# Optimization experiments

Measured on AMD Instinct MI355X. Metric: run time of the kernel, lower is better.

## Reference

```python
import jax, jax.numpy as jnp
import numpy as np

B, N, F_IN, F_OUT = 4, 4096, 64, 64
ALPHA = 0.2  # LeakyReLU negative slope
NEG_INF = -9e15


def setup_inputs() -> dict:
    key = jax.random.key(0)
    k1, k2, k3, k4 = jax.random.split(key, 4)
    h = jax.random.normal(k1, (B, N, F_IN), dtype=jnp.float32)
    adj = jax.random.randint(k2, (B, N, N), 0, 2, dtype=jnp.int32)
    # xavier_uniform-like init (gain 1.414)
    lim_w = 1.414 * np.sqrt(6.0 / (F_IN + F_OUT))
    W = jax.random.uniform(k3, (F_IN, F_OUT), dtype=jnp.float32, minval=-lim_w, maxval=lim_w)
    lim_a = 1.414 * np.sqrt(6.0 / (2 * F_OUT + 1))
    a = jax.random.uniform(k4, (2 * F_OUT, 1), dtype=jnp.float32, minval=-lim_a, maxval=lim_a)
    return {"h": h, "adj": adj, "W": W, "a": a}


def reference(h, adj, W, a):
    # Wh: [B, N, F_out]
    Wh = jnp.matmul(h, W)
    a1 = a[:F_OUT, 0]   # [F_out]
    a2 = a[F_OUT:, 0]   # [F_out]
    # e[b,i,j] = LeakyReLU(Wh[b,i].a1 + Wh[b,j].a2)  (decomposed, avoids O(N^2*2F) concat)
    ei = jnp.einsum('bnf,f->bn', Wh, a1)  # source term
    ej = jnp.einsum('bnf,f->bn', Wh, a2)  # target term
    e = ei[:, :, None] + ej[:, None, :]   # [B, N, N]
    e = jnp.where(e > 0, e, ALPHA * e)    # LeakyReLU
    att = jnp.where(adj > 0, e, NEG_INF)
    att = jax.nn.softmax(att, axis=-1)
    h_prime = jnp.matmul(att, Wh)         # [B, N, F_out]
    return jax.nn.elu(h_prime)
```

## Files before the change

### kernel.cpp

```cpp
#include <hip/hip_runtime.h>
#include <stdint.h>

#define N_NODES 4096
#define F_DIM   64
#define LRELU_ALPHA 0.2f

typedef _Float16 f16;
typedef __attribute__((ext_vector_type(8))) _Float16 half8;
typedef __attribute__((ext_vector_type(4))) float f32x4;

__global__ __launch_bounds__(256) void gat_pp(
    const float* __restrict__ h, const float* __restrict__ W,
    const float* __restrict__ a, const int* __restrict__ adj,
    float* __restrict__ ei, float* __restrict__ ej,
    f16* __restrict__ whB, float* __restrict__ blockmax,
    uint32_t* __restrict__ bits)
{
  __shared__ float sh_h[4][F_DIM];
  __shared__ f16 tile[F_DIM][16];
  __shared__ float wmax[4];
  const int t = threadIdx.x, w = t >> 6, lane = t & 63;

  if (blockIdx.x >= 1024) {
    const int r = blockIdx.x - 1024;
    const int* row = adj + (size_t)r * N_NODES;
    const int jw0 = w * 1024;

    int v[16];
#pragma unroll
    for (int p = 0; p < 16; ++p)
      v[p] = row[jw0 + p * 64 + lane];

#pragma unroll
    for (int p = 0; p < 16; ++p) {
      const unsigned long long m = __ballot(v[p] > 0);
      if (lane == 0)
        *(uint64_t*)(bits + (size_t)r * 128 + ((jw0 + p * 64) >> 5)) = m;
    }
    return;
  }

  const int n0 = blockIdx.x * 16;
  const int b  = n0 >> 12;
  const int nl0 = n0 & (N_NODES - 1);

  float wcol[F_DIM];
#pragma unroll
  for (int k = 0; k < F_DIM; ++k) wcol[k] = W[k * F_DIM + lane];
  const float a1 = a[lane], a2 = a[F_DIM + lane];

  float runmax = -3e38f;
  for (int r = 0; r < 4; ++r) {
    const int loc = w * 4 + r;
    const int n = n0 + loc;
    const float hv = h[(size_t)n * F_DIM + lane];
    sh_h[w][lane] = hv;
    float wh = 0.f;
#pragma unroll
    for (int k = 0; k < F_DIM; k += 4) {
      const float4 hb = *(const float4*)(&sh_h[w][k]);
      wh = fmaf(hb.x, wcol[k + 0], wh);
      wh = fmaf(hb.y, wcol[k + 1], wh);
      wh = fmaf(hb.z, wcol[k + 2], wh);
      wh = fmaf(hb.w, wcol[k + 3], wh);
    }
    float s1 = wh * a1, s2 = wh * a2;
#pragma unroll
    for (int off = 32; off; off >>= 1) {
      s1 += __shfl_xor(s1, off);
      s2 += __shfl_xor(s2, off);
    }
    if (lane == 0) { ei[n] = s1; ej[n] = s2; }
    runmax = fmaxf(runmax, s2);
    tile[lane][loc] = (f16)wh;
  }
  if (lane == 0) wmax[w] = runmax;
  __syncthreads();

  {
    const int jc = nl0 >> 5;
    const int q0 = (nl0 >> 3) & 3;
    const int fc = t >> 6;
    const int r6 = t & 63;
    const int qp = r6 >> 5;
    const int m  = (r6 >> 1) & 15;
    const int xh = (t & 1) * 4;
    const int loc = qp * 8 + xh;
    f16* dst = whB + (((size_t)(b * 128 + jc)) * 4 + fc) * 512
                   + ((q0 + qp) * 16 + m) * 8 + xh;
    *(uint2*)dst = *(const uint2*)(&tile[fc * 16 + m][loc]);
  }
  if (t == 0)
    blockmax[blockIdx.x] =
        fmaxf(fmaxf(wmax[0], wmax[1]), fmaxf(wmax[2], wmax[3]));
}

__global__ __launch_bounds__(512, 6) void gat_attn(
    const uint32_t* __restrict__ bits, const float* __restrict__ ei,
    const float* __restrict__ ej, const f16* __restrict__ whB,
    const float* __restrict__ blockmax, float* __restrict__ out)
{
  __shared__ float num_lds[8][16][F_DIM];
  __shared__ float den_lds[8][16];

  const int t = threadIdx.x, w = t >> 6, lane = t & 63;
  const int quad = lane >> 4, m = lane & 15;
  const int b  = blockIdx.x >> 8;
  const int i0 = (blockIdx.x & 255) * 16;
  const int i  = i0 + m;
  const int rowg = b * N_NODES + i;

  float maxej;
  {
    const float4 v = *(const float4*)(blockmax + b * 256 + lane * 4);
    maxej = fmaxf(fmaxf(v.x, v.y), fmaxf(v.z, v.w));
#pragma unroll
    for (int off = 32; off; off >>= 1)
      maxej = fmaxf(maxej, __shfl_xor(maxej, off));
  }

  const float ei_s = ei[rowg];
  float bnd = ei_s + maxej;
  bnd = fmaxf(bnd, LRELU_ALPHA * bnd);
  const float c1 = ei_s - bnd;
  const float c2 = LRELU_ALPHA * ei_s - bnd;

  const float* ejb     = ej + b * N_NODES;
  const uint32_t* bitrow = bits + (size_t)rowg * 128 + w * 16;
  const f16* whw = whB + ((size_t)(b * 128 + w * 16)) * 2048 + lane * 8;

  f32x4 acc[4] = {{0.f,0.f,0.f,0.f},{0.f,0.f,0.f,0.f},
                  {0.f,0.f,0.f,0.f},{0.f,0.f,0.f,0.f}};
  float den = 0.f;
  const int jbase = w * (N_NODES / 8);

  for (int jo = 0; jo < 4; ++jo) {
    const uint4 dq = *(const uint4*)(bitrow + jo * 4);
    const uint32_t dws[4] = {dq.x, dq.y, dq.z, dq.w};

#pragma unroll
    for (int ji = 0; ji < 4; ++ji) {
      const int jc = jo * 4 + ji;
      const int jk = jbase + jc * 32 + quad * 8;
      const uint32_t dw = dws[ji];

      float ejA[8];
      *(float4*)(&ejA[0]) = *(const float4*)(ejb + jk);
      *(float4*)(&ejA[4]) = *(const float4*)(ejb + jk + 4);

      const f16* wjc = whw + (size_t)jc * 2048;
      half8 bf[4];
#pragma unroll
      for (int fc = 0; fc < 4; ++fc)
        bf[fc] = *(const half8*)(wjc + fc * 512);

      half8 pa;
#pragma unroll
      for (int x = 0; x < 8; ++x) {
        const float arg = fmaxf(ejA[x] + c1, fmaf(LRELU_ALPHA, ejA[x], c2));
        const float p =
            ((dw >> (quad * 8 + x)) & 1u) ? __expf(arg) : 0.f;
        pa[x] = (f16)p;
        den += (float)pa[x];
      }

#pragma unroll
      for (int fc = 0; fc < 4; ++fc)
        acc[fc] = __builtin_amdgcn_mfma_f32_16x16x32_f16(pa, bf[fc], acc[fc], 0, 0, 0);
    }
  }

  den += __shfl_xor(den, 16);
  den += __shfl_xor(den, 32);
  if (lane < 16) den_lds[w][lane] = den;

#pragma unroll
  for (int fc = 0; fc < 4; ++fc)
#pragma unroll
    for (int rg = 0; rg < 4; ++rg)
      num_lds[w][quad * 4 + rg][fc * 16 + m] = acc[fc][rg];
  __syncthreads();

#pragma unroll
  for (int k = 0; k < 2; ++k) {
    const int idx = k * 512 + t;
    const int il = idx >> 6, f = idx & 63;
    float num = 0.f, d = 0.f;
#pragma unroll
    for (int ww = 0; ww < 8; ++ww) {
      num += num_lds[ww][il][f];
      d   += den_lds[ww][il];
    }
    float v = (d > 0.f) ? (num / d) : 0.f;
    v = (v > 0.f) ? v : expm1f(v);
    out[((size_t)(b * N_NODES + i0 + il)) * F_DIM + f] = v;
  }
}

extern "C" void kernel_launch(void* const* d_in, const int* in_sizes, int n_in,
                              void* d_out, int out_size, void* d_ws, size_t ws_size,
                              hipStream_t stream) {
  const float* h   = (const float*)d_in[0];
  const int*   adj = (const int*)d_in[1];
  const float* W   = (const float*)d_in[2];
  const float* a   = (const float*)d_in[3];
  float* out = (float*)d_out;

  char* ws = (char*)d_ws;
  float*    ei       = (float*)ws;
  float*    ej       = (float*)(ws + 65536);
  float*    blockmax = (float*)(ws + 131072);
  f16*      whB      = (f16*)(ws + 135168);
  uint32_t* bits     = (uint32_t*)(ws + 2232320);

  hipLaunchKernelGGL(gat_pp, dim3(17408), dim3(256), 0, stream,
                     h, W, a, adj, ei, ej, whB, blockmax, bits);
  hipLaunchKernelGGL(gat_attn, dim3(1024), dim3(512), 0, stream,
                     bits, ei, ej, whB, blockmax, out);
}
```

Baseline: 400.2 us.

## Process 32 rows per attention block and interleave projection with adjacency packing

```diff
diff --git a/kernel.cpp b/kernel.cpp
--- a/kernel.cpp
+++ b/kernel.cpp
@@ -20,9 +20,11 @@
   __shared__ f16 tile[F_DIM][16];
   __shared__ float wmax[4];
   const int t = threadIdx.x, w = t >> 6, lane = t & 63;
-
-  if (blockIdx.x >= 1024) {
-    const int r = blockIdx.x - 1024;
+  const int bid = blockIdx.x;
+  const int pid = bid / 17;
+
+  if (bid % 17 != 0) {
+    const int r = bid - 1 - pid;
     const int* row = adj + (size_t)r * N_NODES;
     const int jw0 = w * 1024;
 
@@ -40,7 +42,7 @@
     return;
   }
 
-  const int n0 = blockIdx.x * 16;
+  const int n0 = pid * 16;
   const int b  = n0 >> 12;
   const int nl0 = n0 & (N_NODES - 1);
 
@@ -91,24 +93,24 @@
     *(uint2*)dst = *(const uint2*)(&tile[fc * 16 + m][loc]);
   }
   if (t == 0)
-    blockmax[blockIdx.x] =
+    blockmax[pid] =
         fmaxf(fmaxf(wmax[0], wmax[1]), fmaxf(wmax[2], wmax[3]));
 }
 
-__global__ __launch_bounds__(512, 6) void gat_attn(
+__global__ __launch_bounds__(512, 4) void gat_attn(
     const uint32_t* __restrict__ bits, const float* __restrict__ ei,
     const float* __restrict__ ej, const f16* __restrict__ whB,
     const float* __restrict__ blockmax, float* __restrict__ out)
 {
-  __shared__ float num_lds[8][16][F_DIM];
-  __shared__ float den_lds[8][16];
+  __shared__ float num_lds[8][32][F_DIM];
+  __shared__ float den_lds[8][32];
 
   const int t = threadIdx.x, w = t >> 6, lane = t & 63;
   const int quad = lane >> 4, m = lane & 15;
-  const int b  = blockIdx.x >> 8;
-  const int i0 = (blockIdx.x & 255) * 16;
-  const int i  = i0 + m;
-  const int rowg = b * N_NODES + i;
+  const int b  = blockIdx.x >> 7;
+  const int i0 = (blockIdx.x & 127) * 32;
+  const int rowg0 = b * N_NODES + i0 + m;
+  const int rowg1 = rowg0 + 16;
 
   float maxej;
   {
@@ -119,30 +121,37 @@
       maxej = fmaxf(maxej, __shfl_xor(maxej, off));
   }
 
-  const float ei_s = ei[rowg];
-  float bnd = ei_s + maxej;
-  bnd = fmaxf(bnd, LRELU_ALPHA * bnd);
-  const float c1 = ei_s - bnd;
-  const float c2 = LRELU_ALPHA * ei_s - bnd;
-
-  const float* ejb     = ej + b * N_NODES;
-  const uint32_t* bitrow = bits + (size_t)rowg * 128 + w * 16;
+  const float ei0 = ei[rowg0], ei1 = ei[rowg1];
+  float bnd0 = ei0 + maxej;
+  bnd0 = fmaxf(bnd0, LRELU_ALPHA * bnd0);
+  float bnd1 = ei1 + maxej;
+  bnd1 = fmaxf(bnd1, LRELU_ALPHA * bnd1);
+  const float c10 = ei0 - bnd0, c20 = LRELU_ALPHA * ei0 - bnd0;
+  const float c11 = ei1 - bnd1, c21 = LRELU_ALPHA * ei1 - bnd1;
+
+  const float* ejb = ej + b * N_NODES;
+  const uint32_t* bitrow0 = bits + (size_t)rowg0 * 128 + w * 16;
+  const uint32_t* bitrow1 = bits + (size_t)rowg1 * 128 + w * 16;
   const f16* whw = whB + ((size_t)(b * 128 + w * 16)) * 2048 + lane * 8;
 
-  f32x4 acc[4] = {{0.f,0.f,0.f,0.f},{0.f,0.f,0.f,0.f},
-                  {0.f,0.f,0.f,0.f},{0.f,0.f,0.f,0.f}};
-  float den = 0.f;
+  f32x4 acc0[4] = {{0.f,0.f,0.f,0.f},{0.f,0.f,0.f,0.f},
+                   {0.f,0.f,0.f,0.f},{0.f,0.f,0.f,0.f}};
+  f32x4 acc1[4] = {{0.f,0.f,0.f,0.f},{0.f,0.f,0.f,0.f},
+                   {0.f,0.f,0.f,0.f},{0.f,0.f,0.f,0.f}};
+  float den0 = 0.f, den1 = 0.f;
   const int jbase = w * (N_NODES / 8);
 
   for (int jo = 0; jo < 4; ++jo) {
-    const uint4 dq = *(const uint4*)(bitrow + jo * 4);
-    const uint32_t dws[4] = {dq.x, dq.y, dq.z, dq.w};
+    const uint4 dq0 = *(const uint4*)(bitrow0 + jo * 4);
+    const uint4 dq1 = *(const uint4*)(bitrow1 + jo * 4);
+    const uint32_t dws0[4] = {dq0.x, dq0.y, dq0.z, dq0.w};
+    const uint32_t dws1[4] = {dq1.x, dq1.y, dq1.z, dq1.w};
 
 #pragma unroll
     for (int ji = 0; ji < 4; ++ji) {
       const int jc = jo * 4 + ji;
       const int jk = jbase + jc * 32 + quad * 8;
-      const uint32_t dw = dws[ji];
+      const uint32_t dw0 = dws0[ji], dw1 = dws1[ji];
 
       float ejA[8];
       *(float4*)(&ejA[0]) = *(const float4*)(ejb + jk);
@@ -154,35 +163,48 @@
       for (int fc = 0; fc < 4; ++fc)
         bf[fc] = *(const half8*)(wjc + fc * 512);
 
-      half8 pa;
+      half8 pa0, pa1;
 #pragma unroll
       for (int x = 0; x < 8; ++x) {
-        const float arg = fmaxf(ejA[x] + c1, fmaf(LRELU_ALPHA, ejA[x], c2));
-        const float p =
-            ((dw >> (quad * 8 + x)) & 1u) ? __expf(arg) : 0.f;
-        pa[x] = (f16)p;
-        den += (float)pa[x];
+        const float e = ejA[x];
+        const float g0 = fmaxf(e + c10, fmaf(LRELU_ALPHA, e, c20));
+        const float g1 = fmaxf(e + c11, fmaf(LRELU_ALPHA, e, c21));
+        const float p0 = ((dw0 >> (quad * 8 + x)) & 1u) ? __expf(g0) : 0.f;
+        const float p1 = ((dw1 >> (quad * 8 + x)) & 1u) ? __expf(g1) : 0.f;
+        pa0[x] = (f16)p0;
+        pa1[x] = (f16)p1;
+        den0 += (float)pa0[x];
+        den1 += (float)pa1[x];
       }
 
 #pragma unroll
-      for (int fc = 0; fc < 4; ++fc)
-        acc[fc] = __builtin_amdgcn_mfma_f32_16x16x32_f16(pa, bf[fc], acc[fc], 0, 0, 0);
-    }
-  }
-
-  den += __shfl_xor(den, 16);
-  den += __shfl_xor(den, 32);
-  if (lane < 16) den_lds[w][lane] = den;
+      for (int fc = 0; fc < 4; ++fc) {
+        acc0[fc] = __builtin_amdgcn_mfma_f32_16x16x32_f16(pa0, bf[fc], acc0[fc], 0, 0, 0);
+        acc1[fc] = __builtin_amdgcn_mfma_f32_16x16x32_f16(pa1, bf[fc], acc1[fc], 0, 0, 0);
+      }
+    }
+  }
+
+  den0 += __shfl_xor(den0, 16);
+  den0 += __shfl_xor(den0, 32);
+  den1 += __shfl_xor(den1, 16);
+  den1 += __shfl_xor(den1, 32);
+  if (lane < 16) {
+    den_lds[w][lane] = den0;
+    den_lds[w][lane + 16] = den1;
+  }
 
 #pragma unroll
   for (int fc = 0; fc < 4; ++fc)
 #pragma unroll
-    for (int rg = 0; rg < 4; ++rg)
-      num_lds[w][quad * 4 + rg][fc * 16 + m] = acc[fc][rg];
+    for (int rg = 0; rg < 4; ++rg) {
+      num_lds[w][quad * 4 + rg][fc * 16 + m] = acc0[fc][rg];
+      num_lds[w][16 + quad * 4 + rg][fc * 16 + m] = acc1[fc][rg];
+    }
   __syncthreads();
 
 #pragma unroll
-  for (int k = 0; k < 2; ++k) {
+  for (int k = 0; k < 4; ++k) {
     const int idx = k * 512 + t;
     const int il = idx >> 6, f = idx & 63;
     float num = 0.f, d = 0.f;
@@ -215,6 +237,6 @@
 
   hipLaunchKernelGGL(gat_pp, dim3(17408), dim3(256), 0, stream,
                      h, W, a, adj, ei, ej, whB, blockmax, bits);
-  hipLaunchKernelGGL(gat_attn, dim3(1024), dim3(512), 0, stream,
+  hipLaunchKernelGGL(gat_attn, dim3(512), dim3(512), 0, stream,
                      bits, ei, ej, whB, blockmax, out);
 }
```

New measurement: 393.0 us. About the same (-1.8%).

## Split attention over key quarters with LDS-staged Wh and a separate reduction kernel

Applied to the files above, without the earlier changes.

```diff
diff --git a/kernel.cpp b/kernel.cpp
--- a/kernel.cpp
+++ b/kernel.cpp
@@ -20,17 +20,17 @@
   __shared__ f16 tile[F_DIM][16];
   __shared__ float wmax[4];
   const int t = threadIdx.x, w = t >> 6, lane = t & 63;
-
-  if (blockIdx.x >= 1024) {
-    const int r = blockIdx.x - 1024;
+  const int bid = blockIdx.x;
+  const int pid = bid / 17;
+
+  if (bid % 17 != 0) {
+    const int r = bid - 1 - pid;
     const int* row = adj + (size_t)r * N_NODES;
     const int jw0 = w * 1024;
-
     int v[16];
 #pragma unroll
     for (int p = 0; p < 16; ++p)
       v[p] = row[jw0 + p * 64 + lane];
-
 #pragma unroll
     for (int p = 0; p < 16; ++p) {
       const unsigned long long m = __ballot(v[p] > 0);
@@ -40,7 +40,7 @@
     return;
   }
 
-  const int n0 = blockIdx.x * 16;
+  const int n0 = pid * 16;
   const int b  = n0 >> 12;
   const int nl0 = n0 & (N_NODES - 1);
 
@@ -91,24 +91,26 @@
     *(uint2*)dst = *(const uint2*)(&tile[fc * 16 + m][loc]);
   }
   if (t == 0)
-    blockmax[blockIdx.x] =
+    blockmax[pid] =
         fmaxf(fmaxf(wmax[0], wmax[1]), fmaxf(wmax[2], wmax[3]));
 }
 
-__global__ __launch_bounds__(512, 6) void gat_attn(
+__global__ __launch_bounds__(256, 4) void gat_attn(
     const uint32_t* __restrict__ bits, const float* __restrict__ ei,
     const float* __restrict__ ej, const f16* __restrict__ whB,
-    const float* __restrict__ blockmax, float* __restrict__ out)
+    const float* __restrict__ blockmax,
+    float* __restrict__ pnum, float* __restrict__ pden)
 {
-  __shared__ float num_lds[8][16][F_DIM];
-  __shared__ float den_lds[8][16];
+  __shared__ __align__(16) f16 lwh[2][2048];
+  __shared__ __align__(16) float lej[1024];
+  __shared__ uint32_t lbits[64][33];
 
   const int t = threadIdx.x, w = t >> 6, lane = t & 63;
   const int quad = lane >> 4, m = lane & 15;
-  const int b  = blockIdx.x >> 8;
-  const int i0 = (blockIdx.x & 255) * 16;
-  const int i  = i0 + m;
-  const int rowg = b * N_NODES + i;
+  const int jq  = blockIdx.x & 3;
+  const int rcg = blockIdx.x >> 2;
+  const int b   = rcg >> 6;
+  const int growbase = rcg * 64;
 
   float maxej;
   {
@@ -119,82 +121,102 @@
       maxej = fmaxf(maxej, __shfl_xor(maxej, off));
   }
 
+  const int rowg = growbase + w * 16 + m;
   const float ei_s = ei[rowg];
   float bnd = ei_s + maxej;
   bnd = fmaxf(bnd, LRELU_ALPHA * bnd);
   const float c1 = ei_s - bnd;
   const float c2 = LRELU_ALPHA * ei_s - bnd;
 
-  const float* ejb     = ej + b * N_NODES;
-  const uint32_t* bitrow = bits + (size_t)rowg * 128 + w * 16;
-  const f16* whw = whB + ((size_t)(b * 128 + w * 16)) * 2048 + lane * 8;
+#pragma unroll
+  for (int pass = 0; pass < 8; ++pass) {
+    const int r = pass * 8 + (t >> 5);
+    const int dwi = t & 31;
+    lbits[r][dwi] = bits[(size_t)(growbase + r) * 128 + jq * 32 + dwi];
+  }
+  *(float4*)(&lej[t * 4]) =
+      *(const float4*)(ej + b * N_NODES + jq * 1024 + t * 4);
+
+  const f16* whq = whB + ((size_t)(b * 128 + jq * 32)) * 2048;
+  *(half8*)(&lwh[0][t * 8]) = *(const half8*)(whq + t * 8);
+  __syncthreads();
 
   f32x4 acc[4] = {{0.f,0.f,0.f,0.f},{0.f,0.f,0.f,0.f},
                   {0.f,0.f,0.f,0.f},{0.f,0.f,0.f,0.f}};
   float den = 0.f;
-  const int jbase = w * (N_NODES / 8);
-
-  for (int jo = 0; jo < 4; ++jo) {
-    const uint4 dq = *(const uint4*)(bitrow + jo * 4);
-    const uint32_t dws[4] = {dq.x, dq.y, dq.z, dq.w};
-
-#pragma unroll
-    for (int ji = 0; ji < 4; ++ji) {
-      const int jc = jo * 4 + ji;
-      const int jk = jbase + jc * 32 + quad * 8;
-      const uint32_t dw = dws[ji];
-
-      float ejA[8];
-      *(float4*)(&ejA[0]) = *(const float4*)(ejb + jk);
-      *(float4*)(&ejA[4]) = *(const float4*)(ejb + jk + 4);
-
-      const f16* wjc = whw + (size_t)jc * 2048;
-      half8 bf[4];
-#pragma unroll
-      for (int fc = 0; fc < 4; ++fc)
-        bf[fc] = *(const half8*)(wjc + fc * 512);
-
-      half8 pa;
-#pragma unroll
-      for (int x = 0; x < 8; ++x) {
-        const float arg = fmaxf(ejA[x] + c1, fmaf(LRELU_ALPHA, ejA[x], c2));
-        const float p =
-            ((dw >> (quad * 8 + x)) & 1u) ? __expf(arg) : 0.f;
-        pa[x] = (f16)p;
-        den += (float)pa[x];
-      }
-
-#pragma unroll
-      for (int fc = 0; fc < 4; ++fc)
-        acc[fc] = __builtin_amdgcn_mfma_f32_16x16x32_f16(pa, bf[fc], acc[fc], 0, 0, 0);
-    }
+
+  for (int c = 0; c < 32; ++c) {
+    half8 pre;
+    if (c + 1 < 32)
+      pre = *(const half8*)(whq + (size_t)(c + 1) * 2048 + t * 8);
+
+    const int buf = c & 1;
+    const float4 e0 = *(const float4*)(&lej[c * 32 + quad * 8]);
+    const float4 e1 = *(const float4*)(&lej[c * 32 + quad * 8 + 4]);
+    const float ejA[8] = {e0.x, e0.y, e0.z, e0.w, e1.x, e1.y, e1.z, e1.w};
+    const uint32_t dw = lbits[w * 16 + m][c];
+
+    half8 bf[4];
+#pragma unroll
+    for (int fc = 0; fc < 4; ++fc)
+      bf[fc] = *(const half8*)(&lwh[buf][fc * 512 + lane * 8]);
+
+    half8 pa;
+#pragma unroll
+    for (int x = 0; x < 8; ++x) {
+      const float e = ejA[x];
+      const float g = fmaxf(e + c1, fmaf(LRELU_ALPHA, e, c2));
+      const float p = ((dw >> (quad * 8 + x)) & 1u) ? __expf(g) : 0.f;
+      pa[x] = (f16)p;
+      den += (float)pa[x];
+    }
+
+#pragma unroll
+    for (int fc = 0; fc < 4; ++fc)
+      acc[fc] = __builtin_amdgcn_mfma_f32_16x16x32_f16(pa, bf[fc], acc[fc], 0, 0, 0);
+
+    __syncthreads();
+    if (c + 1 < 32)
+      *(half8*)(&lwh[buf ^ 1][t * 8]) = pre;
+    __syncthreads();
   }
 
   den += __shfl_xor(den, 16);
   den += __shfl_xor(den, 32);
-  if (lane < 16) den_lds[w][lane] = den;
+  if (lane < 16)
+    pden[(size_t)jq * 16384 + growbase + w * 16 + lane] = den;
 
 #pragma unroll
   for (int fc = 0; fc < 4; ++fc)
 #pragma unroll
     for (int rg = 0; rg < 4; ++rg)
-      num_lds[w][quad * 4 + rg][fc * 16 + m] = acc[fc][rg];
-  __syncthreads();
-
-#pragma unroll
-  for (int k = 0; k < 2; ++k) {
-    const int idx = k * 512 + t;
-    const int il = idx >> 6, f = idx & 63;
-    float num = 0.f, d = 0.f;
-#pragma unroll
-    for (int ww = 0; ww < 8; ++ww) {
-      num += num_lds[ww][il][f];
-      d   += den_lds[ww][il];
-    }
-    float v = (d > 0.f) ? (num / d) : 0.f;
-    v = (v > 0.f) ? v : expm1f(v);
-    out[((size_t)(b * N_NODES + i0 + il)) * F_DIM + f] = v;
-  }
+      pnum[((size_t)jq * 16384 + growbase + w * 16 + quad * 4 + rg) * F_DIM
+           + fc * 16 + m] = acc[fc][rg];
+}
+
+__global__ __launch_bounds__(256) void gat_red(
+    const float* __restrict__ pnum, const float* __restrict__ pden,
+    float* __restrict__ out)
+{
+  const int idx = blockIdx.x * 256 + threadIdx.x;
+  const int base = idx * 4;
+  const int row = base >> 6, col = base & 63;
+  float4 n = {0.f, 0.f, 0.f, 0.f};
+  float d = 0.f;
+#pragma unroll
+  for (int q = 0; q < 4; ++q) {
+    const float4 v = *(const float4*)(pnum + ((size_t)q * 16384 + row) * F_DIM + col);
+    n.x += v.x; n.y += v.y; n.z += v.z; n.w += v.w;
+    d += pden[(size_t)q * 16384 + row];
+  }
+  const float inv = (d > 0.f) ? (1.f / d) : 0.f;
+  float4 v;
+  v.x = n.x * inv; v.y = n.y * inv; v.z = n.z * inv; v.w = n.w * inv;
+  v.x = (v.x > 0.f) ? v.x : expm1f(v.x);
+  v.y = (v.y > 0.f) ? v.y : expm1f(v.y);
+  v.z = (v.z > 0.f) ? v.z : expm1f(v.z);
+  v.w = (v.w > 0.f) ? v.w : expm1f(v.w);
+  *(float4*)(out + base) = v;
 }
 
 extern "C" void kernel_launch(void* const* d_in, const int* in_sizes, int n_in,
@@ -212,9 +234,13 @@
   float*    blockmax = (float*)(ws + 131072);
   f16*      whB      = (f16*)(ws + 135168);
   uint32_t* bits     = (uint32_t*)(ws + 2232320);
+  float*    pnum     = (float*)(ws + 10620928);
+  float*    pden     = (float*)(ws + 27398144);
 
   hipLaunchKernelGGL(gat_pp, dim3(17408), dim3(256), 0, stream,
                      h, W, a, adj, ei, ej, whB, blockmax, bits);
-  hipLaunchKernelGGL(gat_attn, dim3(1024), dim3(512), 0, stream,
-                     bits, ei, ej, whB, blockmax, out);
-}
+  hipLaunchKernelGGL(gat_attn, dim3(1024), dim3(256), 0, stream,
+                     bits, ei, ej, whB, blockmax, pnum, pden);
+  hipLaunchKernelGGL(gat_red, dim3(1024), dim3(256), 0, stream,
+                     pnum, pden, out);
+}
```

Result: no change. 399.9 us (-0.1%).
